# Kernel tuning notes

Hardware: AMD Instinct MI355X
Metric: run time of the kernel (lower is better)

## Reference

```python
import jax, jax.numpy as jnp
import numpy as np

# Geometry constants (LinearProbeGeom)
N_DET = 128
N_T = 2048
DT_S = 2.5e-08        # 40 MHz sampling
PITCH_M = 3.0e-04
C_M_S = 1540.0
NX, NY = 256, 256
X0_M, DX_M = -0.0192, 1.5e-04
Y0_M, DY_M = 1.0e-03, 1.5e-04
ARRAY_X0_M, ARRAY_Y_M = -0.0192, 0.0
N_FFT = N_T  # fft_pad = 0
EPS = np.float32(np.finfo(np.float32).eps)


def _constants():
    freq = np.fft.rfftfreq(N_FFT, d=DT_S)
    omega = (2.0 * np.pi * freq).astype(np.float32)            # (F,)
    fw = np.ones_like(omega)
    if omega.size > 2:
        fw[1:-1] = 2.0
    if N_FFT % 2 == 0 and omega.size > 1:
        fw[-1] = 1.0
    kx = (2.0 * np.pi * np.fft.fftfreq(N_DET, d=PITCH_M)).astype(np.float32)  # (D,)
    xs = (X0_M + np.arange(NX) * DX_M - ARRAY_X0_M).astype(np.float32)        # (X,)
    ys = (Y0_M + np.arange(NY) * DY_M - ARRAY_Y_M).astype(np.float32)         # (Y,)
    # Hann apodization over detectors (buffer, non-trainable)
    apod = (0.5 - 0.5 * np.cos(2.0 * np.pi * np.arange(N_DET) / max(N_DET - 1, 1))).astype(np.float32)
    return (jnp.asarray(omega), jnp.asarray(fw), jnp.asarray(kx),
            jnp.asarray(xs), jnp.asarray(ys), jnp.asarray(apod))


def setup_inputs() -> dict:
    key = jax.random.key(0)
    sino = jax.random.normal(key, (8, 1, N_DET, N_T), dtype=jnp.float32)
    return {"sino": sino}


def reference(sino):
    omega, fw, kx, xs, ys, apod = _constants()
    B, C, D, T = sino.shape
    # per-(B,C) standardization over (det, time)
    mean = jnp.mean(sino, axis=(-1, -2), keepdims=True)
    sn = sino - mean
    var = jnp.mean(sn * sn, axis=(-1, -2), keepdims=True)
    sn = sn / jnp.sqrt(var + EPS)
    # time window is rectangular (window=None) -> identity
    sw = sn * apod[None, None, :, None]
    # 2D spectrum: rfft over time, fft over detectors
    spec = jnp.fft.rfft(sw, n=N_FFT, axis=-1)          # (B,C,D,F)
    spec = jnp.fft.fft(spec, axis=2)                   # (B,C,D,F)
    # Stolt dispersion: kz^2 = (w/c)^2 - kx^2, clamped
    kz_sq = (omega / C_M_S)[None, :] ** 2 - (kx ** 2)[:, None]   # (D,F)
    kz = jnp.sqrt(jnp.maximum(kz_sq, 0.0))
    prop_mask = (kz_sq > 0.0).astype(jnp.float32)
    # fold propagation mask and frequency weighting into the spectrum
    sf = spec * (prop_mask * fw[None, :])[None, None, :, :]      # (B,C,D,F) complex
    # per-depth phase shift and frequency reduction
    phase_y = jnp.exp(1j * kz[None, :, :] * ys[:, None, None])   # (Y,D,F) complex64
    band = jnp.einsum('bcdf,ydf->bcyd', sf, phase_y)             # (B,C,Y,D)
    # lateral inverse transform via explicit phase matrix
    phase_x = jnp.exp(1j * kx[:, None] * xs[None, :])            # (D,X)
    img = jnp.einsum('bcyd,dx->bcyx', band, phase_x)             # (B,C,Y,X)
    img_mag = jnp.abs(img)
    apod_sum = jnp.maximum(jnp.sum(apod), EPS)
    fw_sum = jnp.maximum(jnp.sum(fw), EPS)
    return img_mag / (apod_sum * fw_sum)
```

## Files before the change

### kernel.cpp

```cpp
#include <hip/hip_runtime.h>
#include <hip/hip_bf16.h>
#include <math.h>

#define NB 8
#define ND 128
#define NT 2048
#define NF 1025
#define NYY 256
#define NXX 256

#define SPEC_BYTES 8396800
#define BAND_PART_BYTES 2097152
#define BANDH_PART_BYTES 1048576
#define ROWSTAT_OFF 0
#define SPECT_OFF  8192
#define SF_OFF     (SPECT_OFF + SPEC_BYTES)
#define BAND_OFF   (SF_OFF + SPEC_BYTES)

typedef short bf16x8 __attribute__((ext_vector_type(8)));
typedef float f32x4 __attribute__((ext_vector_type(4)));

__device__ __forceinline__ unsigned pk2bf(float lo, float hi) {
  __hip_bfloat162 h = __float22bfloat162_rn(make_float2(lo, hi));
  unsigned u;
  __builtin_memcpy(&u, &h, 4);
  return u;
}

__global__ __launch_bounds__(256) void fk_tfft(const float* __restrict__ sino,
                                               float2* __restrict__ specT,
                                               float2* __restrict__ rowstat) {
  const int row = blockIdx.x;
  const int d = row & (ND - 1);
  const int tid = threadIdx.x;
  __shared__ float2 bufA[1024];
  __shared__ float2 bufB[1024];
  __shared__ float2 wsum[4];
  const float ap = (float)(0.5 - 0.5 * cos(6.283185307179586 * (double)d / 127.0));
  const float2* in = (const float2*)(sino + (size_t)row * NT);
  float s = 0.f, q = 0.f;
  for (int i = tid; i < 1024; i += 256) {
    float2 v = in[i];
    s += v.x + v.y;
    q += v.x * v.x + v.y * v.y;
    bufA[i] = make_float2(v.x * ap, v.y * ap);
  }
  #pragma unroll
  for (int o = 32; o > 0; o >>= 1) {
    s += __shfl_down(s, o);
    q += __shfl_down(q, o);
  }
  if ((tid & 63) == 0) wsum[tid >> 6] = make_float2(s, q);
  __syncthreads();
  if (tid == 0) {
    rowstat[row] = make_float2(wsum[0].x + wsum[1].x + wsum[2].x + wsum[3].x,
                               wsum[0].y + wsum[1].y + wsum[2].y + wsum[3].y);
  }
  float2* src = bufA;
  float2* dst = bufB;
  for (int p = 1; p <= 512; p <<= 1) {
    #pragma unroll
    for (int it = 0; it < 2; ++it) {
      int i = tid + it * 256;
      int k = i & (p - 1);
      float2 u = src[i];
      float2 v = src[i + 512];
      float ang = -3.14159265358979323846f * ((float)k / (float)p);
      float sn, cs; __sincosf(ang, &sn, &cs);
      float2 vw = make_float2(v.x * cs - v.y * sn, v.x * sn + v.y * cs);
      int j = ((i - k) << 1) + k;
      dst[j]     = make_float2(u.x + vw.x, u.y + vw.y);
      dst[j + p] = make_float2(u.x - vw.x, u.y - vw.y);
    }
    __syncthreads();
    float2* t = src; src = dst; dst = t;
  }
  float2* out = specT + (size_t)row * NF;
  for (int k = tid; k < 1024; k += 256) {
    float2 zk = src[k];
    float2 zc = src[(1024 - k) & 1023]; zc.y = -zc.y;
    float2 xe = make_float2(0.5f * (zk.x + zc.x), 0.5f * (zk.y + zc.y));
    float ax = zk.x - zc.x, ay = zk.y - zc.y;
    float2 xo = make_float2(0.5f * ay, -0.5f * ax);
    float ang = -3.14159265358979323846f * ((float)k / 1024.0f);
    float sn, cs; __sincosf(ang, &sn, &cs);
    out[k] = make_float2(xe.x + cs * xo.x - sn * xo.y,
                         xe.y + cs * xo.y + sn * xo.x);
  }
  if (tid == 0) {
    float2 z0 = src[0];
    out[1024] = make_float2(z0.x - z0.y, 0.0f);
  }
}

__global__ __launch_bounds__(256) void fk_dfft(const float2* __restrict__ specT,
                                               float2* __restrict__ sf) {
  const int b = blockIdx.y;
  const int f0 = blockIdx.x * 4;
  const int sub = threadIdx.x >> 6;
  const int i = threadIdx.x & 63;
  const int f = f0 + sub;
  const bool valid = (f < NF);
  __shared__ float2 A[4][128];
  __shared__ float2 Bf[4][128];
  if (valid) {
    const float2* col = specT + ((size_t)b * ND) * NF + f;
    A[sub][i]      = col[(size_t)i * NF];
    A[sub][i + 64] = col[(size_t)(i + 64) * NF];
  }
  __syncthreads();
  float2 (*src)[128] = A;
  float2 (*dst)[128] = Bf;
  for (int p = 1; p <= 64; p <<= 1) {
    if (valid) {
      int k = i & (p - 1);
      float2 u = src[sub][i];
      float2 v = src[sub][i + 64];
      float ang = -3.14159265358979323846f * ((float)k / (float)p);
      float sn, cs; __sincosf(ang, &sn, &cs);
      float2 vw = make_float2(v.x * cs - v.y * sn, v.x * sn + v.y * cs);
      int j = ((i - k) << 1) + k;
      dst[sub][j]     = make_float2(u.x + vw.x, u.y + vw.y);
      dst[sub][j + p] = make_float2(u.x - vw.x, u.y - vw.y);
    }
    __syncthreads();
    float2 (*t)[128] = src; src = dst; dst = t;
  }
  if (valid) {
    const float fwv = (f == 0 || f == NF - 1) ? 1.0f : 2.0f;
    double freqd = (double)f / 5.12e-5;
    float omega = (float)(freqd * 6.283185307179586);
    float woc = omega / 1540.0f;
    float woc2 = __fmul_rn(woc, woc);
    #pragma unroll
    for (int h = 0; h < 2; ++h) {
      int kd = i + h * 64;
      int kt = kd < 64 ? kd : kd - 128;
      float kxv = (float)(6.283185307179586 * ((double)kt / 0.0384));
      float kzsq = __fsub_rn(woc2, __fmul_rn(kxv, kxv));
      float m = (kzsq > 0.0f) ? fwv : 0.0f;
      float2 v = src[sub][kd];
      sf[((size_t)(b * ND + kd)) * NF + f] = make_float2(v.x * m, v.y * m);
    }
  }
}

__device__ __forceinline__ unsigned int bf16rne(float x) {
  unsigned int u = __float_as_uint(x);
  return (u + 0x7fffu + ((u >> 16) & 1u)) >> 16;
}

__global__ __launch_bounds__(256, 3) void fk_band_mfma(const float2* __restrict__ sf,
                                                       unsigned int* __restrict__ bandh,
                                                       int flen_base) {
  const int dblk = blockIdx.x;
  const int part = blockIdx.y;
  const int f0 = part * flen_base;
  const int flen = min(flen_base, NF - f0);
  const int tid = threadIdx.x;
  const int lane = tid & 63;
  const int d = dblk * 4 + (tid >> 6);
  const int col = lane & 15;
  const int grp = lane >> 4;

  float kzv[3][4];
  bf16x8 bfr[3], bfi[3];
  #pragma unroll
  for (int kt = 0; kt < 3; ++kt) {
    union { unsigned u[4]; bf16x8 v; } ur, ui;
    #pragma unroll
    for (int c = 0; c < 4; ++c) {
      const int fl = kt * 16 + grp * 4 + c;
      float kv = 0.f;
      float2 s = make_float2(0.f, 0.f);
      if (fl < flen) {
        const int fg = f0 + fl;
        int ktd = d < 64 ? d : d - 128;
        float kxv = (float)(6.283185307179586 * ((double)ktd / 0.0384));
        float kx2 = __fmul_rn(kxv, kxv);
        double freqd = (double)fg / 5.12e-5;
        float omega = (float)(freqd * 6.283185307179586);
        float woc = omega / 1540.0f;
        float kzsq = __fsub_rn(__fmul_rn(woc, woc), kx2);
        kv = (kzsq > 0.0f) ? sqrtf(kzsq) : 0.0f;
        if (col < 8) s = sf[((size_t)(col * ND + d)) * NF + fg];
      }
      kzv[kt][c] = kv;
      ur.u[c] = pk2bf(s.x, -s.y);
      ui.u[c] = pk2bf(s.y,  s.x);
    }
    bfr[kt] = ur.v;
    bfi[kt] = ui.v;
  }

  const float stepf = 2.4e-3f;
  const int arow = lane & 15;
  const f32x4 zz = {0.f, 0.f, 0.f, 0.f};

  #pragma unroll
  for (int h = 0; h < 2; ++h) {
    f32x4 accre[8], accim[8];
    #pragma unroll
    for (int m = 0; m < 8; ++m) { accre[m] = zz; accim[m] = zz; }
    const float yv0 = (float)(1.0e-3 + (double)(h * 128 + arow) * 1.5e-4);
    #pragma unroll
    for (int kt = 0; kt < 3; ++kt) {
      float2 cur[4], stp[4];
      #pragma unroll
      for (int c = 0; c < 4; ++c) {
        float sn, cs;
        __sincosf(kzv[kt][c] * yv0, &sn, &cs);
        cur[c] = make_float2(cs, sn);
        __sincosf(kzv[kt][c] * stepf, &sn, &cs);
        stp[c] = make_float2(cs, sn);
      }
      #pragma unroll
      for (int m = 0; m < 8; ++m) {
        union { unsigned u[4]; bf16x8 v; } ua;
        #pragma unroll
        for (int c = 0; c < 4; ++c) ua.u[c] = pk2bf(cur[c].x, cur[c].y);
        accre[m] = __builtin_amdgcn_mfma_f32_16x16x32_bf16(ua.v, bfr[kt], accre[m], 0, 0, 0);
        accim[m] = __builtin_amdgcn_mfma_f32_16x16x32_bf16(ua.v, bfi[kt], accim[m], 0, 0, 0);
        #pragma unroll
        for (int c = 0; c < 4; ++c) {
          float2 nc;
          nc.x = cur[c].x * stp[c].x - cur[c].y * stp[c].y;
          nc.y = cur[c].x * stp[c].y + cur[c].y * stp[c].x;
          cur[c] = nc;
        }
      }
    }
    if (col < 8) {
      unsigned int* outp = bandh + (size_t)part * (NB * ND * NYY)
                         + ((size_t)(col * ND + d)) * NYY;
      #pragma unroll
      for (int m = 0; m < 8; ++m) {
        const int y0 = h * 128 + m * 16 + grp * 4;
        uint4 pk;
        pk.x = pk2bf(accre[m][0], accim[m][0]);
        pk.y = pk2bf(accre[m][1], accim[m][1]);
        pk.z = pk2bf(accre[m][2], accim[m][2]);
        pk.w = pk2bf(accre[m][3], accim[m][3]);
        *(uint4*)(outp + y0) = pk;
      }
    }
  }
}

__global__ __launch_bounds__(256, 3) void fk_band(const float2* __restrict__ sf,
                                                  unsigned int* __restrict__ bandh,
                                                  int flen_base, int fpad) {
  const int dblk = blockIdx.x;
  const int part = blockIdx.y;
  const int f0 = part * flen_base;
  const int flen = min(flen_base, NF - f0);
  const int tid = threadIdx.x;
  const int w = tid >> 6, l = tid & 63;
  const int d = dblk * 4 + w;
  extern __shared__ float lds[];
  float2* sfs = (float2*)lds;
  float4* kcs = (float4*)(lds + 64 * fpad);
  {
    const int row = tid >> 3;
    const int wr = row >> 3, br = row & 7;
    const int dr = dblk * 4 + wr;
    const float2* srcp = sf + ((size_t)(br * ND + dr)) * NF + f0;
    for (int ff = tid & 7; ff < fpad; ff += 8)
      sfs[row * fpad + ff] = (ff < flen) ? srcp[ff] : make_float2(0.f, 0.f);
  }
  for (int e = tid; e < 4 * fpad; e += 256) {
    const int wk = e / fpad, ff = e - wk * fpad;
    float kzv = 0.f;
    if (ff < flen) {
      int dk = dblk * 4 + wk;
      int kt = dk < 64 ? dk : dk - 128;
      float kxv = (float)(6.283185307179586 * ((double)kt / 0.0384));
      float kx2 = __fmul_rn(kxv, kxv);
      int f = f0 + ff;
      double freqd = (double)f / 5.12e-5;
      float omega = (float)(freqd * 6.283185307179586);
      float woc = omega / 1540.0f;
      float kzsq = __fsub_rn(__fmul_rn(woc, woc), kx2);
      kzv = (kzsq > 0.0f) ? sqrtf(kzsq) : 0.0f;
    }
    float sd, cd;
    __sincosf(kzv * 1.5e-4f, &sd, &cd);
    kcs[e] = make_float4(kzv, cd, sd, 0.f);
  }
  __syncthreads();
  const float y0 = (float)(1.0e-3 + (double)(4 * l) * 1.5e-4);
  float2 acc[8][4];
  #pragma unroll
  for (int b = 0; b < 8; ++b)
    #pragma unroll
    for (int i = 0; i < 4; ++i) acc[b][i] = make_float2(0.f, 0.f);
  const float4* kcw = kcs + w * fpad;
  const float2* rows = sfs + (w * 8) * fpad;
  #pragma unroll 2
  for (int ff = 0; ff < fpad; ++ff) {
    const float4 k4 = kcw[ff];
    float s0, c0;
    __sincosf(k4.x * y0, &s0, &c0);
    float2 ph[4];
    ph[0] = make_float2(c0, s0);
    #pragma unroll
    for (int i = 0; i < 3; ++i)
      ph[i + 1] = make_float2(ph[i].x * k4.y - ph[i].y * k4.z,
                              ph[i].x * k4.z + ph[i].y * k4.y);
    #pragma unroll
    for (int b = 0; b < 8; ++b) {
      float2 p = rows[b * fpad + ff];
      #pragma unroll
      for (int i = 0; i < 4; ++i) {
        acc[b][i].x = fmaf(p.x, ph[i].x, fmaf(-p.y, ph[i].y, acc[b][i].x));
        acc[b][i].y = fmaf(p.x, ph[i].y, fmaf( p.y, ph[i].x, acc[b][i].y));
      }
    }
  }
  unsigned int* outp = bandh + (size_t)part * (NB * ND * NYY);
  #pragma unroll
  for (int b = 0; b < 8; ++b) {
    uint4 pk;
    pk.x = bf16rne(acc[b][0].x) | (bf16rne(acc[b][0].y) << 16);
    pk.y = bf16rne(acc[b][1].x) | (bf16rne(acc[b][1].y) << 16);
    pk.z = bf16rne(acc[b][2].x) | (bf16rne(acc[b][2].y) << 16);
    pk.w = bf16rne(acc[b][3].x) | (bf16rne(acc[b][3].y) << 16);
    ((uint4*)(outp + ((size_t)(b * ND + d)) * NYY))[l] = pk;
  }
}

__global__ __launch_bounds__(256) void fk_sum(const unsigned int* __restrict__ bandh,
                                              float2* __restrict__ bandS, int nparts) {
  const int n = blockIdx.x * 256 + threadIdx.x;
  float sx = 0.f, sy = 0.f;
  for (int p = 0; p < nparts; ++p) {
    unsigned int u = bandh[(size_t)p * (NB * ND * NYY) + n];
    sx += __uint_as_float(u << 16);
    sy += __uint_as_float(u & 0xffff0000u);
  }
  bandS[n] = make_float2(sx, sy);
}

__global__ __launch_bounds__(256) void fk_img(const float2* __restrict__ bandS,
                                              const float2* __restrict__ rowstat,
                                              float* __restrict__ out, float inv_norm) {
  const int y0 = blockIdx.x * 2;
  const int b = blockIdx.y;
  const int tid = threadIdx.x;
  const int half = tid >> 7;
  const int t = tid & 127;
  __shared__ float2 A[2][256];
  __shared__ float2 Bb[2][256];
  __shared__ float2 spart[2];
  {
    float2 v = bandS[((size_t)(b * ND + t)) * NYY + (y0 + half)];
    A[half][t]       = (t < 64)  ? v : make_float2(0.f, 0.f);
    A[half][t + 128] = (t >= 64) ? v : make_float2(0.f, 0.f);
  }
  {
    float2 myrs = make_float2(0.f, 0.f);
    if (tid < 128) myrs = rowstat[b * ND + tid];
    float s = myrs.x, q = myrs.y;
    #pragma unroll
    for (int o = 32; o > 0; o >>= 1) {
      s += __shfl_down(s, o);
      q += __shfl_down(q, o);
    }
    if (tid < 128 && (tid & 63) == 0) spart[tid >> 6] = make_float2(s, q);
  }
  __syncthreads();
  const float nInv = 1.0f / 262144.0f;
  float ssum = spart[0].x + spart[1].x;
  float qsum = spart[0].y + spart[1].y;
  float mean = ssum * nInv;
  float var = qsum * nInv - mean * mean;
  float scl = 1.0f / sqrtf(var + 1.1920928955078125e-7f);

  float2 (*src)[256] = A;
  float2 (*dst)[256] = Bb;
  for (int p = 1; p <= 128; p <<= 1) {
    int i = t;
    int k = i & (p - 1);
    float2 u = src[half][i];
    float2 v = src[half][i + 128];
    float ang = 3.14159265358979323846f * ((float)k / (float)p);
    float sn, cs; __sincosf(ang, &sn, &cs);
    float2 vw = make_float2(v.x * cs - v.y * sn, v.x * sn + v.y * cs);
    int j = ((i - k) << 1) + k;
    dst[half][j]     = make_float2(u.x + vw.x, u.y + vw.y);
    dst[half][j + p] = make_float2(u.x - vw.x, u.y - vw.y);
    __syncthreads();
    float2 (*tt)[256] = src; src = dst; dst = tt;
  }
  float2 r0 = src[0][tid];
  float2 r1 = src[1][tid];
  out[((size_t)b * NYY + y0)     * NXX + tid] = sqrtf(r0.x * r0.x + r0.y * r0.y) * scl * inv_norm;
  out[((size_t)b * NYY + y0 + 1) * NXX + tid] = sqrtf(r1.x * r1.x + r1.y * r1.y) * scl * inv_norm;
}

extern "C" void kernel_launch(void* const* d_in, const int* in_sizes, int n_in,
                              void* d_out, int out_size, void* d_ws, size_t ws_size,
                              hipStream_t stream) {
  const float* sino = (const float*)d_in[0];
  float* out = (float*)d_out;
  char* ws = (char*)d_ws;

  float2*       rowstat = (float2*)(ws + ROWSTAT_OFF);
  float2*       specT   = (float2*)(ws + SPECT_OFF);
  float2*       sf      = (float2*)(ws + SF_OFF);
  unsigned int* bandh   = (unsigned int*)(ws + BAND_OFF);

  double apod_sum = 0.0;
  for (int n = 0; n < ND; ++n) apod_sum += 0.5 - 0.5 * cos(6.283185307179586 * (double)n / 127.0);
  const float inv_norm = (float)(1.0 / (apod_sum * 2048.0));

  fk_tfft<<<NB * ND, 256, 0, stream>>>(sino, specT, rowstat);
  fk_dfft<<<dim3((NF + 3) / 4, NB), 256, 0, stream>>>(specT, sf);

  if (ws_size >= (size_t)BAND_OFF + 24u * BANDH_PART_BYTES + BAND_PART_BYTES) {
    const int FPART = 24;
    const int flen_base = (NF + FPART - 1) / FPART;
    float2* bandS = (float2*)(ws + BAND_OFF + (size_t)FPART * BANDH_PART_BYTES);
    fk_band_mfma<<<dim3(32, FPART), 256, 0, stream>>>(sf, bandh, flen_base);
    fk_sum<<<NB * ND * NYY / 256, 256, 0, stream>>>(bandh, bandS, FPART);
    fk_img<<<dim3(NYY / 2, NB), 256, 0, stream>>>(bandS, rowstat, out, inv_norm);
  } else {
    const int FPART = 8;
    const int flen_base = (NF + FPART - 1) / FPART;
    const int fpad = (flen_base + 1) & ~1;
    const size_t band_lds = (size_t)fpad * 320;
    float2* bandS = (float2*)(ws + BAND_OFF + (size_t)FPART * BANDH_PART_BYTES);
    fk_band<<<dim3(32, FPART), 256, band_lds, stream>>>(sf, bandh, flen_base, fpad);
    fk_sum<<<NB * ND * NYY / 256, 256, 0, stream>>>(bandh, bandS, FPART);
    fk_img<<<dim3(NYY / 2, NB), 256, 0, stream>>>(bandS, rowstat, out, inv_norm);
  }
}
```

Baseline: 63.24 us.

## Split band MFMA over depth halves, halve frequency partitions, vectorize partial sum

The band MFMA kernel now takes the depth half from a third grid dimension instead of looping over both halves. Each block covers twice as many frequencies (6 k-tiles) with 12 partitions instead of 24, so the total grid size is unchanged. The change halves the bf16 partial-sum buffer that fk_sum has to read, and fk_sum now processes two elements per thread with uint2/float4 accesses. In exchange, the spectrum loads and kz/sincos setup are repeated for each depth half, and each thread holds more B-fragment registers, which may lower occupancy.

```diff
diff --git a/kernel.cpp b/kernel.cpp
--- a/kernel.cpp
+++ b/kernel.cpp
@@ -155,6 +155,7 @@
                                                        int flen_base) {
   const int dblk = blockIdx.x;
   const int part = blockIdx.y;
+  const int h    = blockIdx.z;
   const int f0 = part * flen_base;
   const int flen = min(flen_base, NF - f0);
   const int tid = threadIdx.x;
@@ -162,17 +163,39 @@
   const int d = dblk * 4 + (tid >> 6);
   const int col = lane & 15;
   const int grp = lane >> 4;
-
-  float kzv[3][4];
-  bf16x8 bfr[3], bfi[3];
-  #pragma unroll
-  for (int kt = 0; kt < 3; ++kt) {
+  const int arow = lane & 15;
+
+  bf16x8 bfr[6], bfi[6];
+  #pragma unroll
+  for (int kt = 0; kt < 6; ++kt) {
     union { unsigned u[4]; bf16x8 v; } ur, ui;
+    #pragma unroll
+    for (int c = 0; c < 4; ++c) {
+      const int fl = kt * 16 + grp * 4 + c;
+      float2 s = make_float2(0.f, 0.f);
+      if (fl < flen && col < 8) s = sf[((size_t)(col * ND + d)) * NF + f0 + fl];
+      ur.u[c] = pk2bf(s.x, -s.y);
+      ui.u[c] = pk2bf(s.y,  s.x);
+    }
+    bfr[kt] = ur.v;
+    bfi[kt] = ui.v;
+  }
+
+  const float stepf = 2.4e-3f;
+  const f32x4 zz = {0.f, 0.f, 0.f, 0.f};
+  const float yv0 = (float)(1.0e-3 + (double)(h * 128 + arow) * 1.5e-4);
+
+  f32x4 accre[8], accim[8];
+  #pragma unroll
+  for (int m = 0; m < 8; ++m) { accre[m] = zz; accim[m] = zz; }
+
+  #pragma unroll
+  for (int kt = 0; kt < 6; ++kt) {
+    float2 cur[4], stp[4];
     #pragma unroll
     for (int c = 0; c < 4; ++c) {
       const int fl = kt * 16 + grp * 4 + c;
       float kv = 0.f;
-      float2 s = make_float2(0.f, 0.f);
       if (fl < flen) {
         const int fg = f0 + fl;
         int ktd = d < 64 ? d : d - 128;
@@ -183,66 +206,42 @@
         float woc = omega / 1540.0f;
         float kzsq = __fsub_rn(__fmul_rn(woc, woc), kx2);
         kv = (kzsq > 0.0f) ? sqrtf(kzsq) : 0.0f;
-        if (col < 8) s = sf[((size_t)(col * ND + d)) * NF + fg];
       }
-      kzv[kt][c] = kv;
-      ur.u[c] = pk2bf(s.x, -s.y);
-      ui.u[c] = pk2bf(s.y,  s.x);
-    }
-    bfr[kt] = ur.v;
-    bfi[kt] = ui.v;
-  }
-
-  const float stepf = 2.4e-3f;
-  const int arow = lane & 15;
-  const f32x4 zz = {0.f, 0.f, 0.f, 0.f};
-
-  #pragma unroll
-  for (int h = 0; h < 2; ++h) {
-    f32x4 accre[8], accim[8];
-    #pragma unroll
-    for (int m = 0; m < 8; ++m) { accre[m] = zz; accim[m] = zz; }
-    const float yv0 = (float)(1.0e-3 + (double)(h * 128 + arow) * 1.5e-4);
-    #pragma unroll
-    for (int kt = 0; kt < 3; ++kt) {
-      float2 cur[4], stp[4];
+      float sn, cs;
+      __sincosf(kv * yv0, &sn, &cs);
+      cur[c] = make_float2(cs, sn);
+      __sincosf(kv * stepf, &sn, &cs);
+      stp[c] = make_float2(cs, sn);
+    }
+    #pragma unroll
+    for (int m = 0; m < 8; ++m) {
+      union { unsigned u[4]; bf16x8 v; } ua;
+      #pragma unroll
+      for (int c = 0; c < 4; ++c) ua.u[c] = pk2bf(cur[c].x, cur[c].y);
+      accre[m] = __builtin_amdgcn_mfma_f32_16x16x32_bf16(ua.v, bfr[kt], accre[m], 0, 0, 0);
+      accim[m] = __builtin_amdgcn_mfma_f32_16x16x32_bf16(ua.v, bfi[kt], accim[m], 0, 0, 0);
       #pragma unroll
       for (int c = 0; c < 4; ++c) {
-        float sn, cs;
-        __sincosf(kzv[kt][c] * yv0, &sn, &cs);
-        cur[c] = make_float2(cs, sn);
-        __sincosf(kzv[kt][c] * stepf, &sn, &cs);
-        stp[c] = make_float2(cs, sn);
+        float2 nc;
+        nc.x = cur[c].x * stp[c].x - cur[c].y * stp[c].y;
+        nc.y = cur[c].x * stp[c].y + cur[c].y * stp[c].x;
+        cur[c] = nc;
       }
-      #pragma unroll
-      for (int m = 0; m < 8; ++m) {
-        union { unsigned u[4]; bf16x8 v; } ua;
-        #pragma unroll
-        for (int c = 0; c < 4; ++c) ua.u[c] = pk2bf(cur[c].x, cur[c].y);
-        accre[m] = __builtin_amdgcn_mfma_f32_16x16x32_bf16(ua.v, bfr[kt], accre[m], 0, 0, 0);
-        accim[m] = __builtin_amdgcn_mfma_f32_16x16x32_bf16(ua.v, bfi[kt], accim[m], 0, 0, 0);
-        #pragma unroll
-        for (int c = 0; c < 4; ++c) {
-          float2 nc;
-          nc.x = cur[c].x * stp[c].x - cur[c].y * stp[c].y;
-          nc.y = cur[c].x * stp[c].y + cur[c].y * stp[c].x;
-          cur[c] = nc;
-        }
-      }
-    }
-    if (col < 8) {
-      unsigned int* outp = bandh + (size_t)part * (NB * ND * NYY)
-                         + ((size_t)(col * ND + d)) * NYY;
-      #pragma unroll
-      for (int m = 0; m < 8; ++m) {
-        const int y0 = h * 128 + m * 16 + grp * 4;
-        uint4 pk;
-        pk.x = pk2bf(accre[m][0], accim[m][0]);
-        pk.y = pk2bf(accre[m][1], accim[m][1]);
-        pk.z = pk2bf(accre[m][2], accim[m][2]);
-        pk.w = pk2bf(accre[m][3], accim[m][3]);
-        *(uint4*)(outp + y0) = pk;
-      }
+    }
+  }
+
+  if (col < 8) {
+    unsigned int* outp = bandh + (size_t)part * (NB * ND * NYY)
+                       + ((size_t)(col * ND + d)) * NYY;
+    #pragma unroll
+    for (int m = 0; m < 8; ++m) {
+      const int y0 = h * 128 + m * 16 + grp * 4;
+      uint4 pk;
+      pk.x = pk2bf(accre[m][0], accim[m][0]);
+      pk.y = pk2bf(accre[m][1], accim[m][1]);
+      pk.z = pk2bf(accre[m][2], accim[m][2]);
+      pk.w = pk2bf(accre[m][3], accim[m][3]);
+      *(uint4*)(outp + y0) = pk;
     }
   }
 }
@@ -329,16 +328,19 @@
   }
 }
 
-__global__ __launch_bounds__(256) void fk_sum(const unsigned int* __restrict__ bandh,
-                                              float2* __restrict__ bandS, int nparts) {
-  const int n = blockIdx.x * 256 + threadIdx.x;
-  float sx = 0.f, sy = 0.f;
+__global__ __launch_bounds__(256) void fk_sum(const uint2* __restrict__ bandh2,
+                                              float4* __restrict__ bandS4, int nparts) {
+  const int n2 = blockIdx.x * 256 + threadIdx.x;
+  float sx0 = 0.f, sy0 = 0.f, sx1 = 0.f, sy1 = 0.f;
   for (int p = 0; p < nparts; ++p) {
-    unsigned int u = bandh[(size_t)p * (NB * ND * NYY) + n];
-    sx += __uint_as_float(u << 16);
-    sy += __uint_as_float(u & 0xffff0000u);
-  }
-  bandS[n] = make_float2(sx, sy);
+    uint2 u = bandh2[(size_t)p * (NB * ND * NYY / 2) + n2];
+    sx0 += __uint_as_float(u.x << 16);
+    sy0 += __uint_as_float(u.x & 0xffff0000u);
+    sx1 += __uint_as_float(u.y << 16);
+    sy1 += __uint_as_float(u.y & 0xffff0000u);
+  }
+  float4 w; w.x = sx0; w.y = sy0; w.z = sx1; w.w = sy1;
+  bandS4[n2] = w;
 }
 
 __global__ __launch_bounds__(256) void fk_img(const float2* __restrict__ bandS,
@@ -417,12 +419,12 @@
   fk_tfft<<<NB * ND, 256, 0, stream>>>(sino, specT, rowstat);
   fk_dfft<<<dim3((NF + 3) / 4, NB), 256, 0, stream>>>(specT, sf);
 
-  if (ws_size >= (size_t)BAND_OFF + 24u * BANDH_PART_BYTES + BAND_PART_BYTES) {
-    const int FPART = 24;
+  if (ws_size >= (size_t)BAND_OFF + 12u * BANDH_PART_BYTES + BAND_PART_BYTES) {
+    const int FPART = 12;
     const int flen_base = (NF + FPART - 1) / FPART;
     float2* bandS = (float2*)(ws + BAND_OFF + (size_t)FPART * BANDH_PART_BYTES);
-    fk_band_mfma<<<dim3(32, FPART), 256, 0, stream>>>(sf, bandh, flen_base);
-    fk_sum<<<NB * ND * NYY / 256, 256, 0, stream>>>(bandh, bandS, FPART);
+    fk_band_mfma<<<dim3(32, FPART, 2), 256, 0, stream>>>(sf, bandh, flen_base);
+    fk_sum<<<NB * ND * NYY / 512, 256, 0, stream>>>((const uint2*)bandh, (float4*)bandS, FPART);
     fk_img<<<dim3(NYY / 2, NB), 256, 0, stream>>>(bandS, rowstat, out, inv_norm);
   } else {
     const int FPART = 8;
@@ -431,7 +433,7 @@
     const size_t band_lds = (size_t)fpad * 320;
     float2* bandS = (float2*)(ws + BAND_OFF + (size_t)FPART * BANDH_PART_BYTES);
     fk_band<<<dim3(32, FPART), 256, band_lds, stream>>>(sf, bandh, flen_base, fpad);
-    fk_sum<<<NB * ND * NYY / 256, 256, 0, stream>>>(bandh, bandS, FPART);
+    fk_sum<<<NB * ND * NYY / 512, 256, 0, stream>>>((const uint2*)bandh, (float4*)bandS, FPART);
     fk_img<<<dim3(NYY / 2, NB), 256, 0, stream>>>(bandS, rowstat, out, inv_norm);
   }
 }
```

Result: slower. 67.17 us (+6.2%).
